# Performance work log

Measured on AMD Instinct MI355X. Metric: run time of the kernel, lower is better.

Reference implementation:

```python
import jax, jax.numpy as jnp
import numpy as np

INPUT_DIM = 2048
N_FORMULAS = 2048
LITERALS_PER_FORMULA = 16
TOTAL_LITERALS = N_FORMULAS * LITERALS_PER_FORMULA
BINARY_THRESHOLD_EPS = 1.0
ELASTIC_NET_BETA = 0.4


def setup_inputs() -> dict:
    key = jax.random.key(0)
    k1, k2 = jax.random.split(key, 2)
    # learnable mask: original init is eps + 0.5 everywhere; use values in [0, 2]
    # so that the binary threshold at eps=1 is exercised on both sides.
    learnable_mask = jax.random.uniform(k1, (INPUT_DIM, N_FORMULAS), jnp.float32, 0.0, 2.0)
    elastic_net_alpha = jnp.zeros((1,), jnp.float32)
    # per-formula random feature keep mask (Bernoulli, keep_feature_prob ~ 0.5)
    formulas_random_mask = (jax.random.uniform(k2, (INPUT_DIM, N_FORMULAS)) < 0.5).astype(jnp.float32)
    # sparse extension matrix represented as: literal j belongs to formula j // L
    formula_id_per_literal = (jnp.arange(TOTAL_LITERALS, dtype=jnp.int32) // LITERALS_PER_FORMULA)
    return {
        "learnable_mask": learnable_mask,
        "elastic_net_alpha": elastic_net_alpha,
        "formulas_random_mask": formulas_random_mask,
        "formula_id_per_literal": formula_id_per_literal,
    }


def binary_threshold(x, eps):
    # 1.0 where |x| > eps else 0.0 (hard threshold, zero gradient)
    return jnp.where(jnp.abs(x) > eps, jnp.float32(1.0), jnp.float32(0.0))


def reference(learnable_mask, elastic_net_alpha, formulas_random_mask, formula_id_per_literal):
    eps = BINARY_THRESHOLD_EPS
    beta = ELASTIC_NET_BETA
    # number of features kept per formula: [F]
    n_effective_features = jnp.sum(formulas_random_mask, axis=0)
    # diag(matmul(A^T, B)) == einsum('if,if->f') -- same math, no O(F^2) waste
    l2_square_norm_selected = jnp.einsum("if,if->f", jnp.square(learnable_mask), formulas_random_mask)
    l1_norm_selected = jnp.einsum("if,if->f", jnp.abs(learnable_mask), formulas_random_mask)
    l2 = jnp.abs(l2_square_norm_selected / n_effective_features - beta * eps * eps)
    l1 = jnp.abs(l1_norm_selected / n_effective_features - beta * eps)
    sig = jax.nn.sigmoid(elastic_net_alpha[0])
    elastic_net_reg = jnp.mean(l2 * ((1.0 - sig) / 2.0) + l1 * sig)
    # binarize then expand formula columns to literal columns (sparse-dense matmul
    # with a {0,1} selection matrix == column gather)
    learnable_mask_01 = binary_threshold(learnable_mask, eps)
    learnable_binary_mask = jnp.take(learnable_mask_01, formula_id_per_literal, axis=1)  # [D, L_total]
    literals_random_mask = jnp.take(formulas_random_mask, formula_id_per_literal, axis=1)  # [D, L_total]
    return learnable_binary_mask, literals_random_mask, elastic_net_reg
```

## Files before the change

### kernel.cpp

```cpp
#include <hip/hip_runtime.h>
#include <math.h>

#define DIM 2048
#define NF 2048
#define LPF 16
#define LTOT (NF * LPF)
#define BETA 0.4f
#define EPS 1.0f

typedef float f32x4 __attribute__((ext_vector_type(4)));

__global__ void fused_expand_reduce(const float* __restrict__ lm,
                                    const float* __restrict__ frm,
                                    f32x4* __restrict__ out0,
                                    f32x4* __restrict__ out1,
                                    float* __restrict__ ws,
                                    int dch) {
    const int t = threadIdx.x;
    const int f = blockIdx.x * 64 + (t >> 2);
    const int d0 = blockIdx.y * dch;

    float sq = 0.0f, l1 = 0.0f, cnt = 0.0f;
    const size_t obase = (size_t)blockIdx.x * 256 + t;

    #pragma unroll 4
    for (int i = 0; i < dch; ++i) {
        const int d = d0 + i;
        const size_t in_off = ((size_t)d << 11) + f;
        float x = lm[in_off];
        float r = frm[in_off];
        float bin = (fabsf(x) > EPS) ? 1.0f : 0.0f;

        const size_t o = ((size_t)d << 13) + obase;
        f32x4 v0 = { bin, bin, bin, bin };
        f32x4 v1 = { r, r, r, r };
        __builtin_nontemporal_store(v0, &out0[o]);
        __builtin_nontemporal_store(v1, &out1[o]);

        sq  = fmaf(x * x, r, sq);
        l1  = fmaf(fabsf(x), r, l1);
        cnt += r;
    }

    if ((t & 3) == 0) {
        float* w = ws + (size_t)blockIdx.y * 3 * NF;
        w[0 * NF + f] = sq;
        w[1 * NF + f] = l1;
        w[2 * NF + f] = cnt;
    }
}

__global__ void formula_term_kernel(const float* __restrict__ ws,
                                    const float* __restrict__ alpha,
                                    float* __restrict__ ws2,
                                    int ndch) {
    const int f = blockIdx.x * blockDim.x + threadIdx.x;
    float sig = 1.0f / (1.0f + expf(-alpha[0]));
    float w_l2 = (1.0f - sig) * 0.5f;
    float w_l1 = sig;

    float sq = 0.0f, l1 = 0.0f, cnt = 0.0f;
    for (int c = 0; c < ndch; ++c) {
        const float* w = ws + (size_t)c * 3 * NF;
        sq  += w[0 * NF + f];
        l1  += w[1 * NF + f];
        cnt += w[2 * NF + f];
    }
    float l2t = fabsf(sq / cnt - BETA * EPS * EPS);
    float l1t = fabsf(l1 / cnt - BETA * EPS);
    ws2[f] = l2t * w_l2 + l1t * w_l1;
}

__global__ void final_sum_kernel(const float* __restrict__ ws2,
                                 float* __restrict__ out_scalar) {
    __shared__ float red[256];
    const int t = threadIdx.x;
    float total = 0.0f;
    for (int k = 0; k < NF / 256; ++k)
        total += ws2[t + k * 256];
    red[t] = total;
    __syncthreads();
    for (int s = 128; s > 0; s >>= 1) {
        if (t < s) red[t] += red[t + s];
        __syncthreads();
    }
    if (t == 0) out_scalar[0] = red[0] / (float)NF;
}

extern "C" void kernel_launch(void* const* d_in, const int* in_sizes, int n_in,
                              void* d_out, int out_size, void* d_ws, size_t ws_size,
                              hipStream_t stream) {
    const float* lm    = (const float*)d_in[0];
    const float* alpha = (const float*)d_in[1];
    const float* frm   = (const float*)d_in[2];

    float* out = (float*)d_out;
    float* ws  = (float*)d_ws;

    const size_t big = (size_t)DIM * LTOT;
    f32x4* out0 = (f32x4*)out;
    f32x4* out1 = (f32x4*)(out + big);
    float* out_scalar = out + 2 * big;

    int ndch = 64;
    while (ndch > 1 && ((size_t)ndch * 3 * NF + NF) * 4 > ws_size) ndch >>= 1;
    const int dch = DIM / ndch;
    float* ws2 = ws + (size_t)ndch * 3 * NF;

    dim3 grid(NF / 64, ndch);
    fused_expand_reduce<<<grid, 256, 0, stream>>>(lm, frm, out0, out1, ws, dch);
    formula_term_kernel<<<NF / 256, 256, 0, stream>>>(ws, alpha, ws2, ndch);
    final_sum_kernel<<<1, 256, 0, stream>>>(ws2, out_scalar);
}
```

Measured before the change: 132.7 us.

## Split reduction into separate vectorized prefetch kernel before expansion kernel

Moves the per-formula norm reduction out of the expand kernel into its own kernel that reads inputs with 128-bit vector loads and writes partial sums. The expand kernel then only thresholds and writes the two large replicated outputs, ideally finding its inputs in L2/MALL after the prefetch pass. It also hard-codes 64 D-chunks and drops the check against workspace size. The cost is an extra kernel launch and a second read of both 16 MB inputs, in exchange for a leaner store-bound loop.

```diff
diff --git a/kernel.cpp b/kernel.cpp
--- a/kernel.cpp
+++ b/kernel.cpp
@@ -7,24 +7,54 @@
 #define LTOT (NF * LPF)
 #define BETA 0.4f
 #define EPS 1.0f
+#define NDCH 64
+#define DCH (DIM / NDCH)
 
 typedef float f32x4 __attribute__((ext_vector_type(4)));
 
-__global__ void fused_expand_reduce(const float* __restrict__ lm,
-                                    const float* __restrict__ frm,
-                                    f32x4* __restrict__ out0,
-                                    f32x4* __restrict__ out1,
-                                    float* __restrict__ ws,
-                                    int dch) {
+__global__ void reduce_prefetch(const float* __restrict__ lm,
+                                const float* __restrict__ frm,
+                                float* __restrict__ ws) {
+    const int f4 = blockIdx.x * 256 + threadIdx.x;
+    const int d0 = blockIdx.y * DCH;
+
+    const f32x4* lm4 = (const f32x4*)lm;
+    const f32x4* fr4 = (const f32x4*)frm;
+
+    f32x4 sq = {0.f, 0.f, 0.f, 0.f};
+    f32x4 l1 = {0.f, 0.f, 0.f, 0.f};
+    f32x4 cnt = {0.f, 0.f, 0.f, 0.f};
+
+    #pragma unroll 4
+    for (int i = 0; i < DCH; ++i) {
+        const size_t off = ((size_t)(d0 + i) << 9) + f4;
+        f32x4 x = lm4[off];
+        f32x4 r = fr4[off];
+        #pragma unroll
+        for (int j = 0; j < 4; ++j) {
+            sq[j]  = fmaf(x[j] * x[j], r[j], sq[j]);
+            l1[j]  = fmaf(fabsf(x[j]), r[j], l1[j]);
+            cnt[j] += r[j];
+        }
+    }
+
+    float* w = ws + (size_t)blockIdx.y * 3 * NF;
+    ((f32x4*)(w + 0 * NF))[f4] = sq;
+    ((f32x4*)(w + 1 * NF))[f4] = l1;
+    ((f32x4*)(w + 2 * NF))[f4] = cnt;
+}
+
+__global__ void expand_nt(const float* __restrict__ lm,
+                          const float* __restrict__ frm,
+                          f32x4* __restrict__ out0,
+                          f32x4* __restrict__ out1) {
     const int t = threadIdx.x;
     const int f = blockIdx.x * 64 + (t >> 2);
-    const int d0 = blockIdx.y * dch;
-
-    float sq = 0.0f, l1 = 0.0f, cnt = 0.0f;
+    const int d0 = blockIdx.y * DCH;
     const size_t obase = (size_t)blockIdx.x * 256 + t;
 
     #pragma unroll 4
-    for (int i = 0; i < dch; ++i) {
+    for (int i = 0; i < DCH; ++i) {
         const int d = d0 + i;
         const size_t in_off = ((size_t)d << 11) + f;
         float x = lm[in_off];
@@ -36,31 +66,19 @@
         f32x4 v1 = { r, r, r, r };
         __builtin_nontemporal_store(v0, &out0[o]);
         __builtin_nontemporal_store(v1, &out1[o]);
-
-        sq  = fmaf(x * x, r, sq);
-        l1  = fmaf(fabsf(x), r, l1);
-        cnt += r;
-    }
-
-    if ((t & 3) == 0) {
-        float* w = ws + (size_t)blockIdx.y * 3 * NF;
-        w[0 * NF + f] = sq;
-        w[1 * NF + f] = l1;
-        w[2 * NF + f] = cnt;
     }
 }
 
 __global__ void formula_term_kernel(const float* __restrict__ ws,
                                     const float* __restrict__ alpha,
-                                    float* __restrict__ ws2,
-                                    int ndch) {
+                                    float* __restrict__ ws2) {
     const int f = blockIdx.x * blockDim.x + threadIdx.x;
     float sig = 1.0f / (1.0f + expf(-alpha[0]));
     float w_l2 = (1.0f - sig) * 0.5f;
     float w_l1 = sig;
 
     float sq = 0.0f, l1 = 0.0f, cnt = 0.0f;
-    for (int c = 0; c < ndch; ++c) {
+    for (int c = 0; c < NDCH; ++c) {
         const float* w = ws + (size_t)c * 3 * NF;
         sq  += w[0 * NF + f];
         l1  += w[1 * NF + f];
@@ -101,14 +119,14 @@
     f32x4* out0 = (f32x4*)out;
     f32x4* out1 = (f32x4*)(out + big);
     float* out_scalar = out + 2 * big;
+    float* ws2 = ws + (size_t)NDCH * 3 * NF;
 
-    int ndch = 64;
-    while (ndch > 1 && ((size_t)ndch * 3 * NF + NF) * 4 > ws_size) ndch >>= 1;
-    const int dch = DIM / ndch;
-    float* ws2 = ws + (size_t)ndch * 3 * NF;
+    dim3 gridA(NF / 1024, NDCH);
+    reduce_prefetch<<<gridA, 256, 0, stream>>>(lm, frm, ws);
 
-    dim3 grid(NF / 64, ndch);
-    fused_expand_reduce<<<grid, 256, 0, stream>>>(lm, frm, out0, out1, ws, dch);
-    formula_term_kernel<<<NF / 256, 256, 0, stream>>>(ws, alpha, ws2, ndch);
+    dim3 gridB(NF / 64, NDCH);
+    expand_nt<<<gridB, 256, 0, stream>>>(lm, frm, out0, out1);
+
+    formula_term_kernel<<<NF / 256, 256, 0, stream>>>(ws, alpha, ws2);
     final_sum_kernel<<<1, 256, 0, stream>>>(ws2, out_scalar);
 }
```

New measurement: 128.2 us. -3.4%, faster.
